# Kernel optimization log

Hardware: AMD Instinct MI355X
Metric: run time of the kernel (lower is better)

## Reference

```python
import jax, jax.numpy as jnp
import numpy as np

IDIM1, IDIM2, HDIM = 512, 512, 256
EPS = 1e-5

def _layernorm(x, g, b):
    mu = jnp.mean(x, axis=-1, keepdims=True)
    var = jnp.var(x, axis=-1, keepdims=True)
    return (x - mu) * jax.lax.rsqrt(var + EPS) * g + b

def setup_inputs() -> dict:
    key = jax.random.key(0)
    ks = jax.random.split(key, 8)
    B, N, T = 16, 32, 256
    s1 = 1.0 / np.sqrt(IDIM1)
    s2 = 1.0 / np.sqrt(IDIM2)
    s3 = 1.0 / np.sqrt(HDIM)
    return {
        "x1": jax.random.normal(ks[0], (B, N, IDIM1), jnp.float32),
        "x2": jax.random.normal(ks[1], (B, T, IDIM2), jnp.float32),
        "W1": jax.random.uniform(ks[2], (IDIM1, HDIM), jnp.float32, -s1, s1),
        "b1": jax.random.uniform(ks[3], (HDIM,), jnp.float32, -s1, s1),
        "W2": jax.random.uniform(ks[4], (IDIM2, HDIM), jnp.float32, -s2, s2),
        "b2": jax.random.uniform(ks[5], (HDIM,), jnp.float32, -s2, s2),
        "W3": jax.random.uniform(ks[6], (HDIM, HDIM), jnp.float32, -s3, s3),
        "b3": jax.random.uniform(ks[7], (HDIM,), jnp.float32, -s3, s3),
        "g_norm": jnp.ones((HDIM,), jnp.float32),
        "be_norm": jnp.zeros((HDIM,), jnp.float32),
        "g_norm1": jnp.ones((HDIM,), jnp.float32),
        "be_norm1": jnp.zeros((HDIM,), jnp.float32),
    }

def reference(x1, x2, W1, b1, W2, b2, W3, b3, g_norm, be_norm, g_norm1, be_norm1):
    h1 = jax.nn.relu(x1 @ W1 + b1)          # [B,N,H]
    h2 = jax.nn.relu(x2 @ W2 + b2)          # [B,T,H]
    x = h1[:, :, None, :] * h2[:, None, :, :]  # [B,N,T,H] broadcast Hadamard
    x = _layernorm(x, g_norm, be_norm)
    x = x @ W3 + b3
    return jax.nn.relu(_layernorm(x, g_norm1, be_norm1))
```

## Files before the change

### kernel.cpp

```cpp
#include <hip/hip_runtime.h>
#include <hip/hip_bf16.h>
#include <stdint.h>

#define BB 16
#define NN 32
#define TT 256
#define HH 256
#define DD 512
#define EPSF 1e-5f

#define TROWS 16
#define ASTRIDE 264

typedef __attribute__((ext_vector_type(8))) short short8;
typedef __attribute__((ext_vector_type(4))) float floatx4;

__device__ __forceinline__ unsigned short f2bf(float f) {
    union { float f; unsigned u; } v; v.f = f;
    unsigned u = v.u;
    unsigned r = u + 0x7FFFu + ((u >> 16) & 1u);
    return (unsigned short)(r >> 16);
}
__device__ __forceinline__ float bf2f(unsigned short h) {
    union { unsigned u; float f; } v; v.u = ((unsigned)h) << 16;
    return v.f;
}

__global__ __launch_bounds__(256) void prep_kernel(
    const float* __restrict__ x1, const float* __restrict__ x2,
    const float* __restrict__ W1, const float* __restrict__ b1,
    const float* __restrict__ W2, const float* __restrict__ b2,
    const float* __restrict__ W3,
    float* __restrict__ h1, float* __restrict__ h2,
    unsigned short* __restrict__ W3p_hi, unsigned short* __restrict__ W3p_lo)
{
    const int blk = blockIdx.x;
    const int tid = threadIdx.x;

    if (blk >= 1152) {
        const int p  = (blk - 1152) * 256 + tid;
        const int o0 = p * 16;
        unsigned short thi[16], tlo[16];
#pragma unroll
        for (int e = 0; e < 16; ++e) {
            const int o    = o0 + e;
            const int j    = o & 7;
            const int lane = (o >> 3) & 63;
            const int kk   = (o >> 9) & 7;
            const int ct   = o >> 12;
            const int krow = kk * 32 + (lane >> 4) * 8 + j;
            const int col  = ct * 16 + (lane & 15);
            const float w  = W3[krow * HH + col];
            const unsigned short hi = f2bf(w);
            thi[e] = hi;
            tlo[e] = f2bf(w - bf2f(hi));
        }
        unsigned wh[8], wl[8];
#pragma unroll
        for (int e = 0; e < 8; ++e) {
            wh[e] = (unsigned)thi[2 * e] | ((unsigned)thi[2 * e + 1] << 16);
            wl[e] = (unsigned)tlo[2 * e] | ((unsigned)tlo[2 * e + 1] << 16);
        }
        uint4* dh = reinterpret_cast<uint4*>(W3p_hi + o0);
        dh[0] = make_uint4(wh[0], wh[1], wh[2], wh[3]);
        dh[1] = make_uint4(wh[4], wh[5], wh[6], wh[7]);
        uint4* dl = reinterpret_cast<uint4*>(W3p_lo + o0);
        dl[0] = make_uint4(wl[0], wl[1], wl[2], wl[3]);
        dl[1] = make_uint4(wl[4], wl[5], wl[6], wl[7]);
        return;
    }

    __shared__ float xs[8][DD];

    const int rowgrp  = blk >> 1;
    const int colbase = (blk & 1) * 128;

    const float* x; const float* W; const float* bias; float* h; int row0;
    if (rowgrp < 64) { x = x1; W = W1; bias = b1; h = h1; row0 = rowgrp * 8; }
    else             { x = x2; W = W2; bias = b2; h = h2; row0 = (rowgrp - 64) * 8; }

    {
        const float4* xg = reinterpret_cast<const float4*>(x + (size_t)row0 * DD);
        float4* xl = reinterpret_cast<float4*>(&xs[0][0]);
#pragma unroll
        for (int i = 0; i < 4; ++i) xl[tid + 256 * i] = xg[tid + 256 * i];
    }
    __syncthreads();

    const int jj  = tid & 127;
    const int rh  = tid >> 7;
    const int col = colbase + jj;

    float acc[4] = {0.0f, 0.0f, 0.0f, 0.0f};
    const float* Wp = W + col;

    for (int k = 0; k < DD; k += 8) {
        float w[8];
#pragma unroll
        for (int q = 0; q < 8; ++q) w[q] = Wp[(size_t)(k + q) * HH];
#pragma unroll
        for (int r = 0; r < 4; ++r) {
            const float4 xa = *reinterpret_cast<const float4*>(&xs[rh * 4 + r][k]);
            const float4 xb = *reinterpret_cast<const float4*>(&xs[rh * 4 + r][k + 4]);
            float s = acc[r];
            s = fmaf(xa.x, w[0], s); s = fmaf(xa.y, w[1], s);
            s = fmaf(xa.z, w[2], s); s = fmaf(xa.w, w[3], s);
            s = fmaf(xb.x, w[4], s); s = fmaf(xb.y, w[5], s);
            s = fmaf(xb.z, w[6], s); s = fmaf(xb.w, w[7], s);
            acc[r] = s;
        }
    }

    const float bb = bias[col];
#pragma unroll
    for (int r = 0; r < 4; ++r) {
        const float v = acc[r] + bb;
        h[(size_t)(row0 + rh * 4 + r) * HH + col] = v > 0.0f ? v : 0.0f;
    }
}

__global__ __launch_bounds__(256) void fused_mfma_kernel(
    const float* __restrict__ h1, const float* __restrict__ h2,
    const unsigned short* __restrict__ W3p_hi,
    const unsigned short* __restrict__ W3p_lo,
    const float* __restrict__ b3,
    const float* __restrict__ g0, const float* __restrict__ be0,
    const float* __restrict__ g1, const float* __restrict__ be1,
    float* __restrict__ out)
{
    __shared__ __align__(16) unsigned short Ah_s[TROWS * ASTRIDE];
    __shared__ __align__(16) unsigned short Al_s[TROWS * ASTRIDE];
    __shared__ __align__(16) float Ysm[TROWS * HH];

    const int tid  = threadIdx.x;
    const int wave = tid >> 6;
    const int lane = tid & 63;
    const int blk  = blockIdx.x;
    const int tile = blk & 15;
    const int n    = (blk >> 4) & 31;
    const int b    = blk >> 9;

    {
        const float* h1row = h1 + ((size_t)b * NN + n) * HH;
        const float4 h1v  = *reinterpret_cast<const float4*>(h1row + 4 * lane);
        const float4 g0v  = *reinterpret_cast<const float4*>(g0  + 4 * lane);
        const float4 be0v = *reinterpret_cast<const float4*>(be0 + 4 * lane);
        const float* h2b  = h2 + ((size_t)b * TT + tile * TROWS) * HH;

#pragma unroll
        for (int i = 0; i < 4; ++i) {
            const int r = wave * 4 + i;
            float4 v = *reinterpret_cast<const float4*>(h2b + (size_t)r * HH + 4 * lane);
            v.x *= h1v.x; v.y *= h1v.y; v.z *= h1v.z; v.w *= h1v.w;
            float s = v.x + v.y + v.z + v.w;
            float q = v.x * v.x + v.y * v.y + v.z * v.z + v.w * v.w;
#pragma unroll
            for (int off = 32; off >= 1; off >>= 1) {
                s += __shfl_xor(s, off, 64);
                q += __shfl_xor(q, off, 64);
            }
            const float mu  = s * (1.0f / HH);
            const float var = q * (1.0f / HH) - mu * mu;
            const float rs  = rsqrtf(var + EPSF);
            float af[4];
            af[0] = (v.x - mu) * rs * g0v.x + be0v.x;
            af[1] = (v.y - mu) * rs * g0v.y + be0v.y;
            af[2] = (v.z - mu) * rs * g0v.z + be0v.z;
            af[3] = (v.w - mu) * rs * g0v.w + be0v.w;
            ushort4 ahi, alo;
            ahi.x = f2bf(af[0]); alo.x = f2bf(af[0] - bf2f(ahi.x));
            ahi.y = f2bf(af[1]); alo.y = f2bf(af[1] - bf2f(ahi.y));
            ahi.z = f2bf(af[2]); alo.z = f2bf(af[2] - bf2f(ahi.z));
            ahi.w = f2bf(af[3]); alo.w = f2bf(af[3] - bf2f(ahi.w));
            *reinterpret_cast<ushort4*>(&Ah_s[r * ASTRIDE + 4 * lane]) = ahi;
            *reinterpret_cast<ushort4*>(&Al_s[r * ASTRIDE + 4 * lane]) = alo;
        }
    }
    __syncthreads();

    const int m  = lane & 15;
    const int qd = lane >> 4;

    floatx4 acc[4];
#pragma unroll
    for (int ct = 0; ct < 4; ++ct) {
        const float bv = b3[wave * 64 + ct * 16 + m];
        acc[ct][0] = bv; acc[ct][1] = bv; acc[ct][2] = bv; acc[ct][3] = bv;
    }

    for (int kk = 0; kk < 8; ++kk) {
        short8 bh[4], bl[4];
#pragma unroll
        for (int ct = 0; ct < 4; ++ct) {
            const size_t off = ((size_t)((wave * 4 + ct) * 8 + kk) * 64 + lane) * 8;
            bh[ct] = *reinterpret_cast<const short8*>(W3p_hi + off);
            bl[ct] = *reinterpret_cast<const short8*>(W3p_lo + off);
        }
        const int aoff = m * ASTRIDE + kk * 32 + qd * 8;
        const short8 ah = *reinterpret_cast<const short8*>(&Ah_s[aoff]);
        const short8 al = *reinterpret_cast<const short8*>(&Al_s[aoff]);
#pragma unroll
        for (int ct = 0; ct < 4; ++ct) {
            floatx4 c = acc[ct];
            c = __builtin_amdgcn_mfma_f32_16x16x32_bf16(ah, bh[ct], c, 0, 0, 0);
            c = __builtin_amdgcn_mfma_f32_16x16x32_bf16(al, bh[ct], c, 0, 0, 0);
            c = __builtin_amdgcn_mfma_f32_16x16x32_bf16(ah, bl[ct], c, 0, 0, 0);
            acc[ct] = c;
        }
    }

#pragma unroll
    for (int ct = 0; ct < 4; ++ct) {
        const int row = qd * 4;
        const int col = wave * 64 + ct * 16 + m;
#pragma unroll
        for (int reg = 0; reg < 4; ++reg)
            Ysm[(row + reg) * HH + col] = acc[ct][reg];
    }
    __syncthreads();

    {
        const float4 g1v  = *reinterpret_cast<const float4*>(g1  + 4 * lane);
        const float4 be1v = *reinterpret_cast<const float4*>(be1 + 4 * lane);
        float* outb = out + (((size_t)b * NN + n) * TT + tile * TROWS) * HH;

#pragma unroll
        for (int i = 0; i < 4; ++i) {
            const int r = wave * 4 + i;
            const float4 y = *reinterpret_cast<const float4*>(&Ysm[r * HH + 4 * lane]);
            float s = y.x + y.y + y.z + y.w;
            float q = y.x * y.x + y.y * y.y + y.z * y.z + y.w * y.w;
#pragma unroll
            for (int off = 32; off >= 1; off >>= 1) {
                s += __shfl_xor(s, off, 64);
                q += __shfl_xor(q, off, 64);
            }
            const float mu  = s * (1.0f / HH);
            const float var = q * (1.0f / HH) - mu * mu;
            const float rs  = rsqrtf(var + EPSF);
            float4 o;
            o.x = fmaxf((y.x - mu) * rs * g1v.x + be1v.x, 0.0f);
            o.y = fmaxf((y.y - mu) * rs * g1v.y + be1v.y, 0.0f);
            o.z = fmaxf((y.z - mu) * rs * g1v.z + be1v.z, 0.0f);
            o.w = fmaxf((y.w - mu) * rs * g1v.w + be1v.w, 0.0f);
            *reinterpret_cast<float4*>(outb + (size_t)r * HH + 4 * lane) = o;
        }
    }
}

extern "C" void kernel_launch(void* const* d_in, const int* in_sizes, int n_in,
                              void* d_out, int out_size, void* d_ws, size_t ws_size,
                              hipStream_t stream) {
    const float* x1  = (const float*)d_in[0];
    const float* x2  = (const float*)d_in[1];
    const float* W1  = (const float*)d_in[2];
    const float* b1  = (const float*)d_in[3];
    const float* W2  = (const float*)d_in[4];
    const float* b2  = (const float*)d_in[5];
    const float* W3  = (const float*)d_in[6];
    const float* b3  = (const float*)d_in[7];
    const float* g0  = (const float*)d_in[8];
    const float* be0 = (const float*)d_in[9];
    const float* g1  = (const float*)d_in[10];
    const float* be1 = (const float*)d_in[11];
    float* out = (float*)d_out;

    float* h1 = (float*)d_ws;
    float* h2 = h1 + (size_t)BB * NN * HH;
    unsigned short* W3p_hi = (unsigned short*)(h2 + (size_t)BB * TT * HH);
    unsigned short* W3p_lo = W3p_hi + (size_t)HH * HH;

    hipLaunchKernelGGL(prep_kernel, dim3(1168), dim3(256), 0, stream,
                       x1, x2, W1, b1, W2, b2, W3, h1, h2, W3p_hi, W3p_lo);

    hipLaunchKernelGGL(fused_mfma_kernel, dim3(8192), dim3(256), 0, stream,
                       h1, h2, W3p_hi, W3p_lo, b3, g0, be0, g1, be1, out);
}
```

Before: 280.0 us.

## Double rows per block and do second layernorm straight from MFMA registers

Each block now handles 32 T-rows instead of 16, so every W3 fragment loaded from global memory feeds two MFMA row tiles, and the grid is halved. The second layernorm no longer stages the whole output tile in shared memory. Row sums are reduced across lanes with shuffles, combined across waves through a small shared array, and the output is written directly from the accumulators. The trade-off is more accumulator registers, which may lower occupancy, plus output stores that are only 16 lanes wide per row instead of float4-vectorised.

```diff
diff --git a/kernel.cpp b/kernel.cpp
--- a/kernel.cpp
+++ b/kernel.cpp
@@ -9,7 +9,7 @@
 #define DD 512
 #define EPSF 1e-5f
 
-#define TROWS 16
+#define TROWS 32
 #define ASTRIDE 264
 
 typedef __attribute__((ext_vector_type(8))) short short8;
@@ -130,15 +130,16 @@
 {
     __shared__ __align__(16) unsigned short Ah_s[TROWS * ASTRIDE];
     __shared__ __align__(16) unsigned short Al_s[TROWS * ASTRIDE];
-    __shared__ __align__(16) float Ysm[TROWS * HH];
+    __shared__ float2 Spart[TROWS][4];
+    __shared__ float2 LNP[TROWS];
 
     const int tid  = threadIdx.x;
     const int wave = tid >> 6;
     const int lane = tid & 63;
     const int blk  = blockIdx.x;
-    const int tile = blk & 15;
-    const int n    = (blk >> 4) & 31;
-    const int b    = blk >> 9;
+    const int tile = blk & 7;
+    const int n    = (blk >> 3) & 31;
+    const int b    = blk >> 8;
 
     {
         const float* h1row = h1 + ((size_t)b * NN + n) * HH;
@@ -147,9 +148,9 @@
         const float4 be0v = *reinterpret_cast<const float4*>(be0 + 4 * lane);
         const float* h2b  = h2 + ((size_t)b * TT + tile * TROWS) * HH;
 
-#pragma unroll
-        for (int i = 0; i < 4; ++i) {
-            const int r = wave * 4 + i;
+#pragma unroll 2
+        for (int i = 0; i < 8; ++i) {
+            const int r = wave * 8 + i;
             float4 v = *reinterpret_cast<const float4*>(h2b + (size_t)r * HH + 4 * lane);
             v.x *= h1v.x; v.y *= h1v.y; v.z *= h1v.z; v.w *= h1v.w;
             float s = v.x + v.y + v.z + v.w;
@@ -181,13 +182,18 @@
     const int m  = lane & 15;
     const int qd = lane >> 4;
 
-    floatx4 acc[4];
+    floatx4 acc[2][4];
 #pragma unroll
     for (int ct = 0; ct < 4; ++ct) {
         const float bv = b3[wave * 64 + ct * 16 + m];
-        acc[ct][0] = bv; acc[ct][1] = bv; acc[ct][2] = bv; acc[ct][3] = bv;
-    }
-
+#pragma unroll
+        for (int rt = 0; rt < 2; ++rt) {
+            acc[rt][ct][0] = bv; acc[rt][ct][1] = bv;
+            acc[rt][ct][2] = bv; acc[rt][ct][3] = bv;
+        }
+    }
+
+#pragma unroll 2
     for (int kk = 0; kk < 8; ++kk) {
         short8 bh[4], bl[4];
 #pragma unroll
@@ -196,55 +202,92 @@
             bh[ct] = *reinterpret_cast<const short8*>(W3p_hi + off);
             bl[ct] = *reinterpret_cast<const short8*>(W3p_lo + off);
         }
-        const int aoff = m * ASTRIDE + kk * 32 + qd * 8;
-        const short8 ah = *reinterpret_cast<const short8*>(&Ah_s[aoff]);
-        const short8 al = *reinterpret_cast<const short8*>(&Al_s[aoff]);
+#pragma unroll
+        for (int rt = 0; rt < 2; ++rt) {
+            const int aoff = (rt * 16 + m) * ASTRIDE + kk * 32 + qd * 8;
+            const short8 ah = *reinterpret_cast<const short8*>(&Ah_s[aoff]);
+            const short8 al = *reinterpret_cast<const short8*>(&Al_s[aoff]);
+#pragma unroll
+            for (int ct = 0; ct < 4; ++ct) {
+                floatx4 c = acc[rt][ct];
+                c = __builtin_amdgcn_mfma_f32_16x16x32_bf16(ah, bh[ct], c, 0, 0, 0);
+                c = __builtin_amdgcn_mfma_f32_16x16x32_bf16(al, bh[ct], c, 0, 0, 0);
+                c = __builtin_amdgcn_mfma_f32_16x16x32_bf16(ah, bl[ct], c, 0, 0, 0);
+                acc[rt][ct] = c;
+            }
+        }
+    }
+
+    {
+        float ssum[8], qsum[8];
+#pragma unroll
+        for (int rt = 0; rt < 2; ++rt)
+#pragma unroll
+            for (int reg = 0; reg < 4; ++reg) {
+                float s = 0.0f, q = 0.0f;
+#pragma unroll
+                for (int ct = 0; ct < 4; ++ct) {
+                    const float y = acc[rt][ct][reg];
+                    s += y; q = fmaf(y, y, q);
+                }
+                ssum[rt * 4 + reg] = s; qsum[rt * 4 + reg] = q;
+            }
+#pragma unroll
+        for (int off = 1; off < 16; off <<= 1) {
+#pragma unroll
+            for (int e = 0; e < 8; ++e) {
+                ssum[e] += __shfl_xor(ssum[e], off, 64);
+                qsum[e] += __shfl_xor(qsum[e], off, 64);
+            }
+        }
+        if (m == 0) {
+#pragma unroll
+            for (int rt = 0; rt < 2; ++rt)
+#pragma unroll
+                for (int reg = 0; reg < 4; ++reg) {
+                    const int row = rt * 16 + qd * 4 + reg;
+                    Spart[row][wave] = make_float2(ssum[rt * 4 + reg], qsum[rt * 4 + reg]);
+                }
+        }
+    }
+    __syncthreads();
+
+    if (tid < TROWS) {
+        float s = 0.0f, q = 0.0f;
+#pragma unroll
+        for (int w = 0; w < 4; ++w) {
+            const float2 p = Spart[tid][w];
+            s += p.x; q += p.y;
+        }
+        const float mu  = s * (1.0f / HH);
+        const float var = q * (1.0f / HH) - mu * mu;
+        LNP[tid] = make_float2(mu, rsqrtf(var + EPSF));
+    }
+    __syncthreads();
+
+    {
+        const int colb = wave * 64;
+        float g1c[4], be1c[4];
 #pragma unroll
         for (int ct = 0; ct < 4; ++ct) {
-            floatx4 c = acc[ct];
-            c = __builtin_amdgcn_mfma_f32_16x16x32_bf16(ah, bh[ct], c, 0, 0, 0);
-            c = __builtin_amdgcn_mfma_f32_16x16x32_bf16(al, bh[ct], c, 0, 0, 0);
-            c = __builtin_amdgcn_mfma_f32_16x16x32_bf16(ah, bl[ct], c, 0, 0, 0);
-            acc[ct] = c;
-        }
-    }
-
-#pragma unroll
-    for (int ct = 0; ct < 4; ++ct) {
-        const int row = qd * 4;
-        const int col = wave * 64 + ct * 16 + m;
-#pragma unroll
-        for (int reg = 0; reg < 4; ++reg)
-            Ysm[(row + reg) * HH + col] = acc[ct][reg];
-    }
-    __syncthreads();
-
-    {
-        const float4 g1v  = *reinterpret_cast<const float4*>(g1  + 4 * lane);
-        const float4 be1v = *reinterpret_cast<const float4*>(be1 + 4 * lane);
+            g1c[ct]  = g1[colb + ct * 16 + m];
+            be1c[ct] = be1[colb + ct * 16 + m];
+        }
         float* outb = out + (((size_t)b * NN + n) * TT + tile * TROWS) * HH;
 
 #pragma unroll
-        for (int i = 0; i < 4; ++i) {
-            const int r = wave * 4 + i;
-            const float4 y = *reinterpret_cast<const float4*>(&Ysm[r * HH + 4 * lane]);
-            float s = y.x + y.y + y.z + y.w;
-            float q = y.x * y.x + y.y * y.y + y.z * y.z + y.w * y.w;
-#pragma unroll
-            for (int off = 32; off >= 1; off >>= 1) {
-                s += __shfl_xor(s, off, 64);
-                q += __shfl_xor(q, off, 64);
-            }
-            const float mu  = s * (1.0f / HH);
-            const float var = q * (1.0f / HH) - mu * mu;
-            const float rs  = rsqrtf(var + EPSF);
-            float4 o;
-            o.x = fmaxf((y.x - mu) * rs * g1v.x + be1v.x, 0.0f);
-            o.y = fmaxf((y.y - mu) * rs * g1v.y + be1v.y, 0.0f);
-            o.z = fmaxf((y.z - mu) * rs * g1v.z + be1v.z, 0.0f);
-            o.w = fmaxf((y.w - mu) * rs * g1v.w + be1v.w, 0.0f);
-            *reinterpret_cast<float4*>(outb + (size_t)r * HH + 4 * lane) = o;
-        }
+        for (int rt = 0; rt < 2; ++rt)
+#pragma unroll
+            for (int reg = 0; reg < 4; ++reg) {
+                const int row = rt * 16 + qd * 4 + reg;
+                const float2 p = LNP[row];
+#pragma unroll
+                for (int ct = 0; ct < 4; ++ct) {
+                    const float y = acc[rt][ct][reg];
+                    const float o = fmaxf((y - p.x) * p.y * g1c[ct] + be1c[ct], 0.0f);
+                    outb[(size_t)row * HH + colb + ct * 16 + m] = o;
+                }
+            }
     }
 }
 
@@ -273,6 +316,6 @@
     hipLaunchKernelGGL(prep_kernel, dim3(1168), dim3(256), 0, stream,
                        x1, x2, W1, b1, W2, b2, W3, h1, h2, W3p_hi, W3p_lo);
 
-    hipLaunchKernelGGL(fused_mfma_kernel, dim3(8192), dim3(256), 0, stream,
+    hipLaunchKernelGGL(fused_mfma_kernel, dim3(4096), dim3(256), 0, stream,
                        h1, h2, W3p_hi, W3p_lo, b3, g0, be0, g1, be1, out);
 }
```

Result: faster. 254.8 us (-9.0%).
